# Kernel optimization log

Hardware: AMD Instinct MI355X
Metric: run time of the kernel (lower is better)

Reference implementation:

```python
import jax, jax.numpy as jnp
import numpy as np

B, H, S, D = 2, 16, 2048, 64
NEG = -1000000000.0


def setup_inputs() -> dict:
    key = jax.random.key(0)
    kq, kk, kv, km = jax.random.split(key, 4)
    query = jax.random.normal(kq, (B, H, S, D), dtype=jnp.float32)
    k = jax.random.normal(kk, (B, H, S, D), dtype=jnp.float32)
    value = jax.random.normal(kv, (B, H, S, D), dtype=jnp.float32)
    m = jax.random.randint(km, (B, 1, 1, S), 0, 2).astype(jnp.bool_)
    return {"query": query, "key": k, "value": value, "m": m}


def reference(query, key, value, m):
    # scaled dot-product attention; dropout is identity (eval / p effectively off for deterministic baseline)
    scale = 1.0 / jnp.sqrt(jnp.asarray(query.shape[-1], dtype=query.dtype))
    scores = jnp.einsum('bhqd,bhkd->bhqk', query, key) * scale  # [B,H,S,S]
    scores = jnp.where(m, jnp.asarray(NEG, dtype=scores.dtype), scores)
    p_attn = jax.nn.softmax(scores, axis=-1)
    return jnp.einsum('bhqk,bhkd->bhqd', p_attn, value)
```

## Files before the change

kernel.cpp:

```cpp
#include <hip/hip_runtime.h>
#include <hip/hip_bf16.h>

#define S_LEN 2048
#define DH 64
#define C1 0.18033688011112043f
#define MOFF -16.0f
#define MNEG -1.0e9f

typedef float f32x4 __attribute__((ext_vector_type(4)));
typedef short s16x8 __attribute__((ext_vector_type(8)));
typedef unsigned int u32x4 __attribute__((ext_vector_type(4)));

__device__ __forceinline__ ushort f2bf(float x) {
  union { __hip_bfloat16 b; ushort u; } v;
  v.b = __float2bfloat16(x);
  return v.u;
}
__device__ __forceinline__ unsigned int pack2(float lo, float hi) {
  return (unsigned int)f2bf(lo) | ((unsigned int)f2bf(hi) << 16);
}
__device__ __forceinline__ float fexp2(float x) {
#if __has_builtin(__builtin_amdgcn_exp2f)
  return __builtin_amdgcn_exp2f(x);
#else
  return exp2f(x);
#endif
}

__global__ __launch_bounds__(256) void prep_kernel(
    const float* __restrict__ K, const float* __restrict__ V,
    s16x8* __restrict__ dst, int n8,
    const unsigned char* __restrict__ mraw, float* __restrict__ maskp,
    int nmask) {
  const int i = blockIdx.x * 256 + threadIdx.x;
  const float* src = (i < n8) ? K : V;
  const int j = i & (n8 - 1);
  f32x4 x = ((const f32x4*)src)[2 * j];
  f32x4 y = ((const f32x4*)src)[2 * j + 1];
  s16x8 u;
  u[0] = (short)f2bf(x[0]); u[1] = (short)f2bf(x[1]);
  u[2] = (short)f2bf(x[2]); u[3] = (short)f2bf(x[3]);
  u[4] = (short)f2bf(y[0]); u[5] = (short)f2bf(y[1]);
  u[6] = (short)f2bf(y[2]); u[7] = (short)f2bf(y[3]);
  dst[i] = u;

  if (blockIdx.x < 8) {
    __shared__ int flag;
    if (threadIdx.x == 0) flag = 0;
    __syncthreads();
    int any = 0;
    for (int t = threadIdx.x; t < nmask; t += 256)
      if ((t & 3) != 0 && mraw[t] != 0) any = 1;
    if (any) atomicOr(&flag, 1);
    __syncthreads();
    const int u8 = flag;
    const int* mi = (const int*)mraw;
    const int per = nmask >> 3;
    const int base = blockIdx.x * per;
    for (int t = threadIdx.x; t < per; t += 256) {
      int v = u8 ? (int)mraw[base + t] : mi[base + t];
      maskp[base + t] = v ? MNEG : MOFF;
    }
  }
}

__device__ __forceinline__ void stage_k_tile(const ushort* __restrict__ gK,
                                             ushort* ldsbuf, int wv, int lane) {
#pragma unroll
  for (int i = 0; i < 2; ++i) {
    const int s = 64 * i + lane;
    const int r = 16 * wv + (s >> 3);
    const int c = s & 7;
    const ushort* g = gK + r * 64 + 8 * (c ^ (r & 7));
    ushort* l = ldsbuf + wv * 1024 + i * 512;
    __builtin_amdgcn_global_load_lds((const __attribute__((address_space(1))) void*)g,
                                     (__attribute__((address_space(3))) void*)l,
                                     16, 0, 0);
  }
}

__device__ __forceinline__ void write_vt(ushort* vtbuf, int v_k0, int v_d0,
                                         u32x4 a, u32x4 b) {
  const int kc = v_k0 >> 3;
  const int ko = (2 * v_k0) & 15;
#pragma unroll
  for (int j = 0; j < 4; ++j) {
    unsigned lo = __builtin_amdgcn_perm(b[j], a[j], 0x05040100u);
    unsigned hi = __builtin_amdgcn_perm(b[j], a[j], 0x07060302u);
    const int d0 = v_d0 + 2 * j, d1 = d0 + 1;
    *(unsigned*)((char*)vtbuf + 128 * d0 + 16 * (kc ^ (d0 & 7)) + ko) = lo;
    *(unsigned*)((char*)vtbuf + 128 * d1 + 16 * (kc ^ (d1 & 7)) + ko) = hi;
  }
}

__global__ __launch_bounds__(256) void attn2_kernel(
    const float* __restrict__ Qf, const ushort* __restrict__ Kb,
    const ushort* __restrict__ Vb, const float* __restrict__ maskp,
    float* __restrict__ O) {
  __shared__ __align__(16) ushort lds_k[2][64 * 64];
  __shared__ __align__(16) ushort lds_vt[2][64 * 64];
  __shared__ __align__(16) ushort lds_p[4 * 16 * 64];

  const int wg = blockIdx.x;
  const int swz = (wg & 7) * 128 + (wg >> 3);
  const int bh = swz >> 5;
  const int qt = swz & 31;
  const int bb = bh >> 4;

  const float* Qbase = Qf + (size_t)bh * S_LEN * DH + (size_t)qt * 64 * DH;
  const ushort* Kbase = Kb + (size_t)bh * S_LEN * DH;
  const ushort* Vbase = Vb + (size_t)bh * S_LEN * DH;
  const float* mb = maskp + (size_t)bb * S_LEN;
  float* Ob = O + (size_t)bh * S_LEN * DH + (size_t)qt * 64 * DH;

  const int tid = threadIdx.x;
  const int lane = tid & 63;
  const int wv = tid >> 6;
  const int lj = lane & 15;
  const int lg = lane >> 4;
  const int r7 = lj & 7;

  s16x8 qf[2];
  {
    const float* qr = Qbase + (size_t)(wv * 16 + lj) * DH + 8 * lg;
#pragma unroll
    for (int c = 0; c < 2; ++c) {
      f32x4 a = *(const f32x4*)(qr + 32 * c);
      f32x4 b = *(const f32x4*)(qr + 32 * c + 4);
      s16x8 u;
      u[0] = (short)f2bf(a[0] * C1); u[1] = (short)f2bf(a[1] * C1);
      u[2] = (short)f2bf(a[2] * C1); u[3] = (short)f2bf(a[3] * C1);
      u[4] = (short)f2bf(b[0] * C1); u[5] = (short)f2bf(b[1] * C1);
      u[6] = (short)f2bf(b[2] * C1); u[7] = (short)f2bf(b[3] * C1);
      qf[c] = u;
    }
  }

  f32x4 oacc[4];
#pragma unroll
  for (int dt = 0; dt < 4; ++dt) oacc[dt] = (f32x4){0.f, 0.f, 0.f, 0.f};
  float ps_acc = 0.0f;

  char* pw = (char*)(lds_p + wv * 1024);
  int off_r[2], off_w[4];
#pragma unroll
  for (int c = 0; c < 2; ++c) off_r[c] = 128 * lj + 16 * ((lg + 4 * c) ^ r7);
#pragma unroll
  for (int t = 0; t < 4; ++t)
    off_w[t] = 128 * lj + 16 * ((2 * t + (lg >> 1)) ^ r7) + 8 * (lg & 1);

  const int v_k0 = 2 * (tid & 31);
  const int v_d0 = (tid >> 5) * 8;

  f32x4 mnA[4], mnB[4];
  u32x4 va = {0, 0, 0, 0}, vb = {0, 0, 0, 0};

#pragma unroll
  for (int t = 0; t < 4; ++t) mnA[t] = *(const f32x4*)(mb + 16 * t + 4 * lg);
  stage_k_tile(Kbase, &lds_k[0][0], wv, lane);
  {
    const ushort* s0 = Vbase + (size_t)v_k0 * DH + v_d0;
    va = *(const u32x4*)s0;
    vb = *(const u32x4*)(s0 + DH);
    write_vt(&lds_vt[0][0], v_k0, v_d0, va, vb);
  }
  __syncthreads();

  auto body = [&](int kv, int cb, f32x4 (&mnc)[4], f32x4 (&mnn)[4]) {
    const int nx = kv + 64;
    const bool has = nx < S_LEN;
    if (has) {
#pragma unroll
      for (int t = 0; t < 4; ++t)
        mnn[t] = *(const f32x4*)(mb + nx + 16 * t + 4 * lg);
      stage_k_tile(Kbase + (size_t)nx * DH, &lds_k[cb ^ 1][0], wv, lane);
      const ushort* s0 = Vbase + (size_t)(nx + v_k0) * DH + v_d0;
      va = *(const u32x4*)s0;
      vb = *(const u32x4*)(s0 + DH);
    }

    f32x4 st[4];
#pragma unroll
    for (int t = 0; t < 4; ++t) st[t] = mnc[t];
    const char* kb = (const char*)&lds_k[cb][0];
#pragma unroll
    for (int t = 0; t < 4; ++t) {
      s16x8 kf0 = *(const s16x8*)(kb + 2048 * t + off_r[0]);
      st[t] = __builtin_amdgcn_mfma_f32_16x16x32_bf16(kf0, qf[0], st[t], 0, 0, 0);
      s16x8 kf1 = *(const s16x8*)(kb + 2048 * t + off_r[1]);
      st[t] = __builtin_amdgcn_mfma_f32_16x16x32_bf16(kf1, qf[1], st[t], 0, 0, 0);
    }

#pragma unroll
    for (int t = 0; t < 4; ++t) {
      float p0 = fexp2(st[t][0]);
      float p1 = fexp2(st[t][1]);
      float p2 = fexp2(st[t][2]);
      float p3 = fexp2(st[t][3]);
      ps_acc += (p0 + p1) + (p2 + p3);
      *(unsigned*)(pw + off_w[t]) = pack2(p0, p1);
      *(unsigned*)(pw + off_w[t] + 4) = pack2(p2, p3);
    }
    asm volatile("s_waitcnt lgkmcnt(0)" ::: "memory");
    __builtin_amdgcn_sched_barrier(0);

    const char* vtb = (const char*)&lds_vt[cb][0];
#pragma unroll
    for (int c = 0; c < 2; ++c) {
      s16x8 pf = *(const s16x8*)(pw + off_r[c]);
#pragma unroll
      for (int dt = 0; dt < 4; ++dt) {
        s16x8 vf = *(const s16x8*)(vtb + 2048 * dt + off_r[c]);
        oacc[dt] = __builtin_amdgcn_mfma_f32_16x16x32_bf16(vf, pf, oacc[dt], 0, 0, 0);
      }
    }

    if (has) write_vt(&lds_vt[cb ^ 1][0], v_k0, v_d0, va, vb);
    __syncthreads();
  };

  for (int kv = 0; kv < S_LEN; kv += 128) {
    body(kv, 0, mnA, mnB);
    body(kv + 64, 1, mnB, mnA);
  }

  ps_acc += __shfl_xor(ps_acc, 16);
  ps_acc += __shfl_xor(ps_acc, 32);
  const float inv = 1.0f / ps_acc;

  float* orow = Ob + (size_t)(wv * 16 + lj) * DH;
#pragma unroll
  for (int dt = 0; dt < 4; ++dt) {
    f32x4 v = oacc[dt];
    v[0] *= inv; v[1] *= inv; v[2] *= inv; v[3] *= inv;
    *(f32x4*)(orow + 16 * dt + 4 * lg) = v;
  }
}

extern "C" void kernel_launch(void* const* d_in, const int* in_sizes, int n_in,
                              void* d_out, int out_size, void* d_ws, size_t ws_size,
                              hipStream_t stream) {
  const float* Q = (const float*)d_in[0];
  const float* K = (const float*)d_in[1];
  const float* V = (const float*)d_in[2];
  const unsigned char* M = (const unsigned char*)d_in[3];
  float* Obuf = (float*)d_out;
  const int nmask = in_sizes[3];

  const size_t nelem = (size_t)2 * 16 * S_LEN * DH;
  ushort* kvb = (ushort*)d_ws;
  float* maskp = (float*)((char*)d_ws + 2 * nelem * sizeof(ushort));
  const int n8 = (int)(nelem / 8);

  hipLaunchKernelGGL(prep_kernel, dim3(2 * n8 / 256), dim3(256), 0, stream,
                     K, V, (s16x8*)kvb, n8, M, maskp, nmask);
  hipLaunchKernelGGL(attn2_kernel, dim3(1024), dim3(256), 0, stream,
                     Q, kvb, kvb + nelem, maskp, Obuf);
}
```

Baseline: 170.1 us.

## Use 128-query tiles with 8 waves per block sharing K/V staging

Each workgroup now covers 128 query rows with 8 waves instead of 64 rows with 4 waves, so every staged K and V tile in LDS is reused by twice as many waves. This halves global K/V traffic per query and splits the staging work across 512 threads. Wave priority is raised around the MFMA sections via s_setprio so matrix work is favoured while other waves load. Only 512 blocks are launched, and each barrier now waits for 8 waves, which may hurt latency hiding on a GPU with many CUs.

```diff
diff --git a/kernel.cpp b/kernel.cpp
--- a/kernel.cpp
+++ b/kernel.cpp
@@ -9,7 +9,7 @@
 
 typedef float f32x4 __attribute__((ext_vector_type(4)));
 typedef short s16x8 __attribute__((ext_vector_type(8)));
-typedef unsigned int u32x4 __attribute__((ext_vector_type(4)));
+typedef unsigned int u32x2 __attribute__((ext_vector_type(2)));
 
 __device__ __forceinline__ ushort f2bf(float x) {
   union { __hip_bfloat16 b; ushort u; } v;
@@ -64,27 +64,24 @@
   }
 }
 
-__device__ __forceinline__ void stage_k_tile(const ushort* __restrict__ gK,
-                                             ushort* ldsbuf, int wv, int lane) {
-#pragma unroll
-  for (int i = 0; i < 2; ++i) {
-    const int s = 64 * i + lane;
-    const int r = 16 * wv + (s >> 3);
-    const int c = s & 7;
-    const ushort* g = gK + r * 64 + 8 * (c ^ (r & 7));
-    ushort* l = ldsbuf + wv * 1024 + i * 512;
-    __builtin_amdgcn_global_load_lds((const __attribute__((address_space(1))) void*)g,
-                                     (__attribute__((address_space(3))) void*)l,
-                                     16, 0, 0);
-  }
-}
-
-__device__ __forceinline__ void write_vt(ushort* vtbuf, int v_k0, int v_d0,
-                                         u32x4 a, u32x4 b) {
+__device__ __forceinline__ void stage_k_tile8(const ushort* __restrict__ gK,
+                                              ushort* ldsbuf, int wv, int lane) {
+  const int rs = lane >> 3;
+  const int r = 8 * wv + rs;
+  const int c = lane & 7;
+  const ushort* g = gK + r * 64 + 8 * (c ^ rs);
+  ushort* l = ldsbuf + wv * 512;
+  __builtin_amdgcn_global_load_lds((const __attribute__((address_space(1))) void*)g,
+                                   (__attribute__((address_space(3))) void*)l,
+                                   16, 0, 0);
+}
+
+__device__ __forceinline__ void write_vt4(ushort* vtbuf, int v_k0, int v_d0,
+                                          u32x2 a, u32x2 b) {
   const int kc = v_k0 >> 3;
   const int ko = (2 * v_k0) & 15;
 #pragma unroll
-  for (int j = 0; j < 4; ++j) {
+  for (int j = 0; j < 2; ++j) {
     unsigned lo = __builtin_amdgcn_perm(b[j], a[j], 0x05040100u);
     unsigned hi = __builtin_amdgcn_perm(b[j], a[j], 0x07060302u);
     const int d0 = v_d0 + 2 * j, d1 = d0 + 1;
@@ -93,25 +90,25 @@
   }
 }
 
-__global__ __launch_bounds__(256) void attn2_kernel(
+__global__ __launch_bounds__(512) void attn3_kernel(
     const float* __restrict__ Qf, const ushort* __restrict__ Kb,
     const ushort* __restrict__ Vb, const float* __restrict__ maskp,
     float* __restrict__ O) {
   __shared__ __align__(16) ushort lds_k[2][64 * 64];
   __shared__ __align__(16) ushort lds_vt[2][64 * 64];
-  __shared__ __align__(16) ushort lds_p[4 * 16 * 64];
+  __shared__ __align__(16) ushort lds_p[8 * 16 * 64];
 
   const int wg = blockIdx.x;
-  const int swz = (wg & 7) * 128 + (wg >> 3);
-  const int bh = swz >> 5;
-  const int qt = swz & 31;
+  const int swz = (wg & 7) * 64 + (wg >> 3);
+  const int bh = swz >> 4;
+  const int qt = swz & 15;
   const int bb = bh >> 4;
 
-  const float* Qbase = Qf + (size_t)bh * S_LEN * DH + (size_t)qt * 64 * DH;
+  const float* Qbase = Qf + (size_t)bh * S_LEN * DH + (size_t)qt * 128 * DH;
   const ushort* Kbase = Kb + (size_t)bh * S_LEN * DH;
   const ushort* Vbase = Vb + (size_t)bh * S_LEN * DH;
   const float* mb = maskp + (size_t)bb * S_LEN;
-  float* Ob = O + (size_t)bh * S_LEN * DH + (size_t)qt * 64 * DH;
+  float* Ob = O + (size_t)bh * S_LEN * DH + (size_t)qt * 128 * DH;
 
   const int tid = threadIdx.x;
   const int lane = tid & 63;
@@ -150,19 +147,19 @@
     off_w[t] = 128 * lj + 16 * ((2 * t + (lg >> 1)) ^ r7) + 8 * (lg & 1);
 
   const int v_k0 = 2 * (tid & 31);
-  const int v_d0 = (tid >> 5) * 8;
+  const int v_d0 = (tid >> 5) * 4;
 
   f32x4 mnA[4], mnB[4];
-  u32x4 va = {0, 0, 0, 0}, vb = {0, 0, 0, 0};
+  u32x2 va = {0, 0}, vb = {0, 0};
 
 #pragma unroll
   for (int t = 0; t < 4; ++t) mnA[t] = *(const f32x4*)(mb + 16 * t + 4 * lg);
-  stage_k_tile(Kbase, &lds_k[0][0], wv, lane);
+  stage_k_tile8(Kbase, &lds_k[0][0], wv, lane);
   {
     const ushort* s0 = Vbase + (size_t)v_k0 * DH + v_d0;
-    va = *(const u32x4*)s0;
-    vb = *(const u32x4*)(s0 + DH);
-    write_vt(&lds_vt[0][0], v_k0, v_d0, va, vb);
+    va = *(const u32x2*)s0;
+    vb = *(const u32x2*)(s0 + DH);
+    write_vt4(&lds_vt[0][0], v_k0, v_d0, va, vb);
   }
   __syncthreads();
 
@@ -173,16 +170,17 @@
 #pragma unroll
       for (int t = 0; t < 4; ++t)
         mnn[t] = *(const f32x4*)(mb + nx + 16 * t + 4 * lg);
-      stage_k_tile(Kbase + (size_t)nx * DH, &lds_k[cb ^ 1][0], wv, lane);
+      stage_k_tile8(Kbase + (size_t)nx * DH, &lds_k[cb ^ 1][0], wv, lane);
       const ushort* s0 = Vbase + (size_t)(nx + v_k0) * DH + v_d0;
-      va = *(const u32x4*)s0;
-      vb = *(const u32x4*)(s0 + DH);
+      va = *(const u32x2*)s0;
+      vb = *(const u32x2*)(s0 + DH);
     }
 
     f32x4 st[4];
 #pragma unroll
     for (int t = 0; t < 4; ++t) st[t] = mnc[t];
     const char* kb = (const char*)&lds_k[cb][0];
+    __builtin_amdgcn_s_setprio(1);
 #pragma unroll
     for (int t = 0; t < 4; ++t) {
       s16x8 kf0 = *(const s16x8*)(kb + 2048 * t + off_r[0]);
@@ -190,6 +188,7 @@
       s16x8 kf1 = *(const s16x8*)(kb + 2048 * t + off_r[1]);
       st[t] = __builtin_amdgcn_mfma_f32_16x16x32_bf16(kf1, qf[1], st[t], 0, 0, 0);
     }
+    __builtin_amdgcn_s_setprio(0);
 
 #pragma unroll
     for (int t = 0; t < 4; ++t) {
@@ -205,6 +204,7 @@
     __builtin_amdgcn_sched_barrier(0);
 
     const char* vtb = (const char*)&lds_vt[cb][0];
+    __builtin_amdgcn_s_setprio(1);
 #pragma unroll
     for (int c = 0; c < 2; ++c) {
       s16x8 pf = *(const s16x8*)(pw + off_r[c]);
@@ -214,8 +214,9 @@
         oacc[dt] = __builtin_amdgcn_mfma_f32_16x16x32_bf16(vf, pf, oacc[dt], 0, 0, 0);
       }
     }
-
-    if (has) write_vt(&lds_vt[cb ^ 1][0], v_k0, v_d0, va, vb);
+    __builtin_amdgcn_s_setprio(0);
+
+    if (has) write_vt4(&lds_vt[cb ^ 1][0], v_k0, v_d0, va, vb);
     __syncthreads();
   };
 
@@ -254,6 +255,6 @@
 
   hipLaunchKernelGGL(prep_kernel, dim3(2 * n8 / 256), dim3(256), 0, stream,
                      K, V, (s16x8*)kvb, n8, M, maskp, nmask);
-  hipLaunchKernelGGL(attn2_kernel, dim3(1024), dim3(256), 0, stream,
+  hipLaunchKernelGGL(attn3_kernel, dim3(512), dim3(512), 0, stream,
                      Q, kvb, kvb + nelem, maskp, Obuf);
 }
```

New measurement: 157.7 us. 1.08x faster.
